# Performance work log

Hardware: AMD Instinct MI355X
Metric: run time of the kernel (lower is better)

The kernel has to match this reference:

```python
import jax, jax.numpy as jnp
import numpy as np

NEG_SLOPE = 0.2  # PyG GATv2Conv default
HEADS = 3


def setup_inputs() -> dict:
    key = jax.random.key(0)
    ks = jax.random.split(key, 5)
    N, D, H, C = 16384, 128, HEADS, 128
    x = jax.random.normal(ks[0], (N, D), dtype=jnp.float32)
    Wl = jax.random.normal(ks[1], (D, H * C), dtype=jnp.float32) * (1.0 / np.sqrt(D))
    Wr = jax.random.normal(ks[2], (D, H * C), dtype=jnp.float32) * (1.0 / np.sqrt(D))
    att = jax.random.normal(ks[3], (H, C), dtype=jnp.float32) * (1.0 / np.sqrt(C))
    bias = jnp.zeros((C,), dtype=jnp.float32)
    return {"x": x, "Wl": Wl, "Wr": Wr, "att": att, "bias": bias, "k": 16}


def _knn_indices(x, k):
    # squared euclidean pairwise distances, exclude self (loop=False)
    sq = jnp.sum(x * x, axis=1)
    dist = sq[:, None] + sq[None, :] - 2.0 * (x @ x.T)  # [N, N]
    n = x.shape[0]
    ar = jnp.arange(n)
    dist = dist.at[ar, ar].set(jnp.inf)
    _, idx = jax.lax.top_k(-dist, k)  # [N, k] neighbor (source) indices per target node
    return idx


def reference(x, Wl, Wr, att, bias, k):
    N = x.shape[0]
    H = att.shape[0]
    C = att.shape[1]
    idx = _knn_indices(x, k)                     # [N, k]
    xl = (x @ Wl).reshape(N, H, C)               # source transform
    xr = (x @ Wr).reshape(N, H, C)               # target transform
    xl_nbr = xl[idx]                             # [N, k, H, C] gathered source feats
    g = jax.nn.leaky_relu(xl_nbr + xr[:, None], NEG_SLOPE)
    e = jnp.einsum('nkhc,hc->nkh', g, att)       # per-edge attention logits
    alpha = jax.nn.softmax(e, axis=1)            # softmax over the k neighbors of each target
    out = jnp.einsum('nkh,nkhc->nhc', alpha, xl_nbr)
    return out.mean(axis=1) + bias               # concat=False: mean over heads, then bias
```

## Files before the change

### kernel.cpp

```cpp
#include <hip/hip_runtime.h>
#include <math.h>

#define N_NODES 16384
#define DIM 128
#define HC 384
#define NEG_SLOPE 0.2f
#define KNN 16
#define KP2 10
#define NSEG 4
#define NCAND 160
#define SEGC (N_NODES / NSEG)
#define TILES64 (SEGC / 64)
#define LROW 272
#define LBUF64 (64 * LROW)

typedef _Float16 f16x8 __attribute__((ext_vector_type(8)));
typedef _Float16 f16x2 __attribute__((ext_vector_type(2)));
typedef float f32x4 __attribute__((ext_vector_type(4)));
typedef unsigned long long u64;

__global__ __launch_bounds__(256) void prep_x(const float* __restrict__ x,
                                              float* __restrict__ sq,
                                              _Float16* __restrict__ xhi,
                                              _Float16* __restrict__ xlo) {
  const int wv = threadIdx.x >> 6;
  const int lane = threadIdx.x & 63;
  const int row = blockIdx.x * 4 + wv;
  const float2 v = *(const float2*)&x[row * DIM + lane * 2];
  float s = v.x * v.x + v.y * v.y;
  #pragma unroll
  for (int off = 32; off > 0; off >>= 1) s += __shfl_down(s, off);
  _Float16 h0 = (_Float16)v.x, h1 = (_Float16)v.y;
  _Float16 l0 = (_Float16)(v.x - (float)h0), l1 = (_Float16)(v.y - (float)h1);
  f16x2 hh; hh[0] = h0; hh[1] = h1;
  f16x2 ll; ll[0] = l0; ll[1] = l1;
  *(f16x2*)&xhi[row * DIM + lane * 2] = hh;
  *(f16x2*)&xlo[row * DIM + lane * 2] = ll;
  if (lane == 0) sq[row] = s;
}

__global__ __launch_bounds__(256) void prep_w(const float* __restrict__ Wl,
                                              const float* __restrict__ Wr,
                                              _Float16* __restrict__ wthi,
                                              _Float16* __restrict__ wtlo) {
  const int t = blockIdx.x * 256 + threadIdx.x;
  const int mat = t / 49152;
  const int e = t - mat * 49152;
  const int k = e / HC;
  const int c = e - k * HC;
  const float w = (mat ? Wr : Wl)[e];
  _Float16 h = (_Float16)w;
  _Float16 l = (_Float16)(w - (float)h);
  wthi[mat * 49152 + c * DIM + k] = h;
  wtlo[mat * 49152 + c * DIM + k] = l;
}

__global__ __launch_bounds__(256) void gemm_xw_mfma(const _Float16* __restrict__ xhi,
                                                    const _Float16* __restrict__ xlo,
                                                    const _Float16* __restrict__ wthi,
                                                    const _Float16* __restrict__ wtlo,
                                                    _Float16* __restrict__ xl,
                                                    _Float16* __restrict__ xr) {
  const int lane = threadIdx.x & 63;
  const int wid = blockIdx.x * 4 + (threadIdx.x >> 6);
  const int mat = wid / 6144;
  const int rem = wid - mat * 6144;
  const int rt = rem / 6;
  const int ctg = rem - rt * 6;
  const int r0 = lane & 15;
  const int g8 = (lane >> 4) * 8;

  const _Float16* ap_hi = xhi + (size_t)(rt * 16 + r0) * DIM + g8;
  const _Float16* ap_lo = xlo + (size_t)(rt * 16 + r0) * DIM + g8;
  f16x8 ah[4], al[4];
  #pragma unroll
  for (int ks = 0; ks < 4; ks++) {
    ah[ks] = *(const f16x8*)(ap_hi + ks * 32);
    al[ks] = *(const f16x8*)(ap_lo + ks * 32);
  }
  _Float16* o = mat ? xr : xl;

  #pragma unroll
  for (int ct4 = 0; ct4 < 4; ct4++) {
    const int ct = ctg * 4 + ct4;
    const _Float16* bp_hi = wthi + mat * 49152 + (ct * 16 + r0) * DIM + g8;
    const _Float16* bp_lo = wtlo + mat * 49152 + (ct * 16 + r0) * DIM + g8;
    f32x4 acc = {0.f, 0.f, 0.f, 0.f};
    #pragma unroll
    for (int ks = 0; ks < 4; ks++) {
      f16x8 bh = *(const f16x8*)(bp_hi + ks * 32);
      f16x8 bl = *(const f16x8*)(bp_lo + ks * 32);
      acc = __builtin_amdgcn_mfma_f32_16x16x32_f16(ah[ks], bh, acc, 0, 0, 0);
      acc = __builtin_amdgcn_mfma_f32_16x16x32_f16(ah[ks], bl, acc, 0, 0, 0);
      acc = __builtin_amdgcn_mfma_f32_16x16x32_f16(al[ks], bh, acc, 0, 0, 0);
    }
    #pragma unroll
    for (int i = 0; i < 4; i++) {
      const int row = rt * 16 + (lane >> 4) * 4 + i;
      o[(size_t)row * HC + ct * 16 + r0] = (_Float16)acc[i];
    }
  }
}

__device__ __forceinline__ unsigned umin32(unsigned a, unsigned b) { return a < b ? a : b; }
__device__ __forceinline__ unsigned umax32(unsigned a, unsigned b) { return a > b ? a : b; }

__device__ __forceinline__ void ripple(unsigned pk, unsigned* pool) {
  unsigned cur = pk;
  #pragma unroll
  for (int s = 0; s < KP2; s++) {
    const unsigned mn = umin32(cur, pool[s]);
    cur = umax32(cur, pool[s]);
    pool[s] = mn;
  }
}

__device__ __forceinline__ void insert4s(const f32x4 acc, const f32x4 scv,
                                         int cb_cg, int selfid, unsigned* pool) {
  unsigned k0, k1, k2, k3;
  {
    unsigned kk[4];
    #pragma unroll
    for (int r = 0; r < 4; r++) {
      const int cid = cb_cg + r;
      const float key = fmaf(-2.f, acc[r], scv[r]);
      unsigned u = __float_as_uint(key);
      u ^= (unsigned)(((int)u >> 31) | 0x80000000u);
      unsigned pk = (u & 0xFFFFC000u) | (unsigned)cid;
      kk[r] = (cid == selfid) ? 0xFFFFFFFFu : pk;
    }
    k0 = kk[0]; k1 = kk[1]; k2 = kk[2]; k3 = kk[3];
  }
  #define CSWAP(a, b) { const unsigned mn = umin32(a, b), mx = umax32(a, b); a = mn; b = mx; }
  CSWAP(k0, k1) CSWAP(k2, k3) CSWAP(k0, k2) CSWAP(k1, k3) CSWAP(k1, k2)
  #undef CSWAP
  ripple(k0, pool);
  if (k1 < pool[KP2 - 1]) {
    ripple(k1, pool);
    ripple(k2, pool);
    ripple(k3, pool);
  }
}

__global__ __launch_bounds__(256) void knn_kernel(const _Float16* __restrict__ xhi,
                                                  const float* __restrict__ sq,
                                                  int* __restrict__ cand) {
  __shared__ __align__(16) char lds[2 * LBUF64];

  const int lane = threadIdx.x & 63;
  const int w = threadIdx.x >> 6;
  const int seg = __builtin_amdgcn_readfirstlane(blockIdx.x & 3);
  const int rowgroup = __builtin_amdgcn_readfirstlane((blockIdx.x >> 2) * 4 + w);
  const int rowbase = rowgroup * 16;
  const int segbase = seg * SEGC;
  const int r0 = lane & 15;
  const int g8 = (lane >> 4) * 8;
  const int cg4 = (lane >> 4) * 4;
  const int selfid = rowbase + r0;

  const int st_row = 4 * w + (lane >> 4);
  const int st_chunk = lane & 15;
  size_t st_src[4];
  char* st_dst[4];
  #pragma unroll
  for (int k = 0; k < 4; k++) {
    st_src[k] = (size_t)(st_row + 16 * k) * DIM + st_chunk * 8;
    st_dst[k] = &lds[(st_row + 16 * k) * LROW + st_chunk * 16];
  }

  f16x8 b[4];
  {
    const size_t rb = (size_t)(rowbase + r0) * DIM + g8;
    #pragma unroll
    for (int ks = 0; ks < 4; ks++) b[ks] = *(const f16x8*)&xhi[rb + ks * 32];
  }

  unsigned pool[KP2];
  #pragma unroll
  for (int j = 0; j < KP2; j++) pool[j] = 0xFFFFFFFFu;

  {
    const size_t tb = (size_t)segbase * DIM;
    #pragma unroll
    for (int k = 0; k < 4; k++)
      *(float4*)(st_dst[k]) = *(const float4*)&xhi[tb + st_src[k]];
  }
  f32x4 sA[4];
  #pragma unroll
  for (int s = 0; s < 4; s++) sA[s] = *(const f32x4*)&sq[segbase + 16 * s + cg4];
  __syncthreads();

  int cur = 0;
  for (int t = 0; t < TILES64; t++) {
    const int tn = (t + 1) & (TILES64 - 1);
    const size_t nb = (size_t)(segbase + tn * 64) * DIM;
    float4 g[4];
    #pragma unroll
    for (int k = 0; k < 4; k++) g[k] = *(const float4*)&xhi[nb + st_src[k]];
    f32x4 sN[4];
    #pragma unroll
    for (int s = 0; s < 4; s++) sN[s] = *(const f32x4*)&sq[segbase + tn * 64 + 16 * s + cg4];

    const int cb = segbase + t * 64;
    #pragma unroll
    for (int pr = 0; pr < 2; pr++) {
      const int s0 = pr * 2, s1 = pr * 2 + 1;
      const char* rb0 = &lds[cur * LBUF64 + (16 * s0 + r0) * LROW + g8 * 2];
      const char* rb1 = &lds[cur * LBUF64 + (16 * s1 + r0) * LROW + g8 * 2];
      f16x8 a0[4], a1[4];
      #pragma unroll
      for (int ks = 0; ks < 4; ks++) {
        a0[ks] = *(const f16x8*)(rb0 + ks * 64);
        a1[ks] = *(const f16x8*)(rb1 + ks * 64);
      }
      f32x4 acc0 = {0.f, 0.f, 0.f, 0.f};
      f32x4 acc1 = {0.f, 0.f, 0.f, 0.f};
      #pragma unroll
      for (int ks = 0; ks < 4; ks++) {
        acc0 = __builtin_amdgcn_mfma_f32_16x16x32_f16(a0[ks], b[ks], acc0, 0, 0, 0);
        acc1 = __builtin_amdgcn_mfma_f32_16x16x32_f16(a1[ks], b[ks], acc1, 0, 0, 0);
      }
      insert4s(acc0, sA[s0], cb + 16 * s0 + cg4, selfid, pool);
      insert4s(acc1, sA[s1], cb + 16 * s1 + cg4, selfid, pool);
    }

    #pragma unroll
    for (int k = 0; k < 4; k++)
      *(float4*)(st_dst[k] + (cur ^ 1) * LBUF64) = g[k];
    __syncthreads();
    #pragma unroll
    for (int s = 0; s < 4; s++) sA[s] = sN[s];
    cur ^= 1;
  }

  const int row = rowbase + r0;
  int* dst = cand + (size_t)row * NCAND + ((lane >> 4) * NSEG + seg) * KP2;
  #pragma unroll
  for (int e = 0; e < KP2; e++) dst[e] = (int)(pool[e] & 0x3FFFu);
}

__device__ __forceinline__ unsigned flip32(float f) {
  unsigned u = __float_as_uint(f);
  return u ^ (unsigned)(((int)u >> 31) | 0x80000000u);
}
__device__ __forceinline__ u64 umin64(u64 a, u64 b) { return a < b ? a : b; }

__global__ __launch_bounds__(256) void refine_kernel(const float* __restrict__ x,
                                                     const float* __restrict__ sq,
                                                     const int* __restrict__ cand,
                                                     int* __restrict__ idxo) {
  __shared__ __align__(16) float Xrow[4][DIM];
  __shared__ u64 Keys[4][NCAND];
  const int wv = threadIdx.x >> 6;
  const int lane = threadIdx.x & 63;
  const int row = blockIdx.x * 4 + wv;

  {
    const float2 v = *(const float2*)&x[(size_t)row * DIM + lane * 2];
    *(float2*)&Xrow[wv][lane * 2] = v;
  }

  const int cs = lane >> 3;
  const int ch8 = lane & 7;
  const int base = row * NCAND;
  const float sr = sq[row];

  #pragma nounroll
  for (int it = 0; it < 20; it++) {
    const int ci = it * 8 + cs;
    const int c = cand[base + ci];
    const float4* p = (const float4*)&x[(size_t)c * DIM];
    float d = 0.f;
    #pragma unroll
    for (int j = 0; j < 4; j++) {
      const float4 a = p[ch8 + 8 * j];
      const float4 xv = *(const float4*)&Xrow[wv][(ch8 + 8 * j) * 4];
      d += xv.x * a.x + xv.y * a.y + xv.z * a.z + xv.w * a.w;
    }
    d += __shfl_xor(d, 1);
    d += __shfl_xor(d, 2);
    d += __shfl_xor(d, 4);
    if (ch8 == 0) {
      const float dist = sr + sq[c] - 2.f * d;
      Keys[wv][ci] = ((u64)flip32(dist) << 32) | (unsigned)c;
    }
  }

  u64 k0 = Keys[wv][lane];
  u64 k1 = Keys[wv][64 + lane];
  u64 k2 = (lane < 32) ? Keys[wv][128 + lane] : ~0ull;

  int* dst = idxo + (size_t)row * KNN;
  #pragma unroll
  for (int e = 0; e < KNN; e++) {
    u64 m = umin64(k0, umin64(k1, k2));
    #pragma unroll
    for (int off = 32; off > 0; off >>= 1) {
      const u64 o = __shfl_xor(m, off);
      m = umin64(m, o);
    }
    if (k0 == m)      { dst[e] = (int)(unsigned)m; k0 = ~0ull; }
    else if (k1 == m) { dst[e] = (int)(unsigned)m; k1 = ~0ull; }
    else if (k2 == m) { dst[e] = (int)(unsigned)m; k2 = ~0ull; }
  }
}

__global__ __launch_bounds__(256) void attn_kernel(const _Float16* __restrict__ xl,
                                                   const _Float16* __restrict__ xr,
                                                   const float* __restrict__ att,
                                                   const float* __restrict__ bias,
                                                   const int* __restrict__ idxo,
                                                   float* __restrict__ out) {
  const int n = blockIdx.x * 4 + (threadIdx.x >> 6);
  const int lane = threadIdx.x & 63;
  const int ch = lane * 2;
  int myn = 0;
  if (lane < KNN) myn = idxo[(size_t)n * KNN + lane];
  float o0 = 0.f, o1 = 0.f;
  #pragma unroll
  for (int h = 0; h < 3; h++) {
    const f16x2 rr = *(const f16x2*)&xr[(size_t)n * HC + h * 128 + ch];
    const float r0 = (float)rr[0], r1 = (float)rr[1];
    const float2 av = *(const float2*)&att[h * 128 + ch];
    float v0[KNN], v1[KNN], e[KNN];
    #pragma unroll
    for (int kk = 0; kk < KNN; kk++) {
      const f16x2 xv = *(const f16x2*)&xl[(size_t)__shfl(myn, kk) * HC + h * 128 + ch];
      const float x0 = (float)xv[0], x1 = (float)xv[1];
      v0[kk] = x0; v1[kk] = x1;
      float g0 = x0 + r0; g0 = g0 >= 0.f ? g0 : NEG_SLOPE * g0;
      float g1 = x1 + r1; g1 = g1 >= 0.f ? g1 : NEG_SLOPE * g1;
      float p = av.x * g0 + av.y * g1;
      #pragma unroll
      for (int off = 32; off > 0; off >>= 1) p += __shfl_xor(p, off);
      e[kk] = p;
    }
    float m = e[0];
    #pragma unroll
    for (int kk = 1; kk < KNN; kk++) m = fmaxf(m, e[kk]);
    float s = 0.f;
    float w[KNN];
    #pragma unroll
    for (int kk = 0; kk < KNN; kk++) { w[kk] = expf(e[kk] - m); s += w[kk]; }
    #pragma unroll
    for (int kk = 0; kk < KNN; kk++) {
      const float al = w[kk] / s;
      o0 += al * v0[kk];
      o1 += al * v1[kk];
    }
  }
  const float2 bv = *(const float2*)&bias[ch];
  float2 ov;
  ov.x = o0 / 3.f + bv.x;
  ov.y = o1 / 3.f + bv.y;
  *(float2*)&out[(size_t)n * 128 + ch] = ov;
}

extern "C" void kernel_launch(void* const* d_in, const int* in_sizes, int n_in,
                              void* d_out, int out_size, void* d_ws, size_t ws_size,
                              hipStream_t stream) {
  const float* x    = (const float*)d_in[0];
  const float* Wl   = (const float*)d_in[1];
  const float* Wr   = (const float*)d_in[2];
  const float* att  = (const float*)d_in[3];
  const float* bias = (const float*)d_in[4];
  float* out = (float*)d_out;

  _Float16* xhi  = (_Float16*)d_ws;
  _Float16* xlo  = xhi + (size_t)N_NODES * DIM;
  _Float16* wthi = xlo + (size_t)N_NODES * DIM;
  _Float16* wtlo = wthi + 2 * HC * DIM;
  _Float16* xl   = wtlo + 2 * HC * DIM;
  _Float16* xr   = xl + (size_t)N_NODES * HC;
  float*    sqv  = (float*)(xr + (size_t)N_NODES * HC);
  int*      cnd  = (int*)(sqv + N_NODES);
  int*      idx  = cnd + (size_t)N_NODES * NCAND;

  prep_x<<<N_NODES / 4, 256, 0, stream>>>(x, sqv, xhi, xlo);
  prep_w<<<384, 256, 0, stream>>>(Wl, Wr, wthi, wtlo);
  gemm_xw_mfma<<<3072, 256, 0, stream>>>(xhi, xlo, wthi, wtlo, xl, xr);
  knn_kernel<<<N_NODES / 16, 256, 0, stream>>>(xhi, sqv, cnd);
  refine_kernel<<<N_NODES / 4, 256, 0, stream>>>(x, sqv, cnd, idx);
  attn_kernel<<<N_NODES / 4, 256, 0, stream>>>(xl, xr, att, bias, idx, out);
}
```

Measured before the change: 421.3 us.

## Register-block KNN over two row tiles per wave and share A-fragments in projection GEMM

```diff
diff --git a/kernel.cpp b/kernel.cpp
--- a/kernel.cpp
+++ b/kernel.cpp
@@ -6,9 +6,9 @@
 #define HC 384
 #define NEG_SLOPE 0.2f
 #define KNN 16
-#define KP2 10
-#define NSEG 4
-#define NCAND 160
+#define KP2 6
+#define NSEG 8
+#define NCAND 192
 #define SEGC (N_NODES / NSEG)
 #define TILES64 (SEGC / 64)
 #define LROW 272
@@ -63,10 +63,8 @@
                                                     _Float16* __restrict__ xr) {
   const int lane = threadIdx.x & 63;
   const int wid = blockIdx.x * 4 + (threadIdx.x >> 6);
-  const int mat = wid / 6144;
-  const int rem = wid - mat * 6144;
-  const int rt = rem / 6;
-  const int ctg = rem - rt * 6;
+  const int rt = wid / 6;
+  const int ctg = wid - rt * 6;
   const int r0 = lane & 15;
   const int g8 = (lane >> 4) * 8;
 
@@ -78,26 +76,29 @@
     ah[ks] = *(const f16x8*)(ap_hi + ks * 32);
     al[ks] = *(const f16x8*)(ap_lo + ks * 32);
   }
-  _Float16* o = mat ? xr : xl;
-
-  #pragma unroll
-  for (int ct4 = 0; ct4 < 4; ct4++) {
-    const int ct = ctg * 4 + ct4;
-    const _Float16* bp_hi = wthi + mat * 49152 + (ct * 16 + r0) * DIM + g8;
-    const _Float16* bp_lo = wtlo + mat * 49152 + (ct * 16 + r0) * DIM + g8;
-    f32x4 acc = {0.f, 0.f, 0.f, 0.f};
-    #pragma unroll
-    for (int ks = 0; ks < 4; ks++) {
-      f16x8 bh = *(const f16x8*)(bp_hi + ks * 32);
-      f16x8 bl = *(const f16x8*)(bp_lo + ks * 32);
-      acc = __builtin_amdgcn_mfma_f32_16x16x32_f16(ah[ks], bh, acc, 0, 0, 0);
-      acc = __builtin_amdgcn_mfma_f32_16x16x32_f16(ah[ks], bl, acc, 0, 0, 0);
-      acc = __builtin_amdgcn_mfma_f32_16x16x32_f16(al[ks], bh, acc, 0, 0, 0);
-    }
-    #pragma unroll
-    for (int i = 0; i < 4; i++) {
-      const int row = rt * 16 + (lane >> 4) * 4 + i;
-      o[(size_t)row * HC + ct * 16 + r0] = (_Float16)acc[i];
+
+  #pragma unroll
+  for (int mat = 0; mat < 2; mat++) {
+    _Float16* o = mat ? xr : xl;
+    #pragma unroll
+    for (int ct4 = 0; ct4 < 4; ct4++) {
+      const int ct = ctg * 4 + ct4;
+      const _Float16* bp_hi = wthi + mat * 49152 + (ct * 16 + r0) * DIM + g8;
+      const _Float16* bp_lo = wtlo + mat * 49152 + (ct * 16 + r0) * DIM + g8;
+      f32x4 acc = {0.f, 0.f, 0.f, 0.f};
+      #pragma unroll
+      for (int ks = 0; ks < 4; ks++) {
+        f16x8 bh = *(const f16x8*)(bp_hi + ks * 32);
+        f16x8 bl = *(const f16x8*)(bp_lo + ks * 32);
+        acc = __builtin_amdgcn_mfma_f32_16x16x32_f16(ah[ks], bh, acc, 0, 0, 0);
+        acc = __builtin_amdgcn_mfma_f32_16x16x32_f16(ah[ks], bl, acc, 0, 0, 0);
+        acc = __builtin_amdgcn_mfma_f32_16x16x32_f16(al[ks], bh, acc, 0, 0, 0);
+      }
+      #pragma unroll
+      for (int i = 0; i < 4; i++) {
+        const int row = rt * 16 + (lane >> 4) * 4 + i;
+        o[(size_t)row * HC + ct * 16 + r0] = (_Float16)acc[i];
+      }
     }
   }
 }
@@ -142,21 +143,22 @@
   }
 }
 
-__global__ __launch_bounds__(256) void knn_kernel(const _Float16* __restrict__ xhi,
-                                                  const float* __restrict__ sq,
-                                                  int* __restrict__ cand) {
+__global__ __launch_bounds__(256, 4) void knn_kernel(const _Float16* __restrict__ xhi,
+                                                     const float* __restrict__ sq,
+                                                     int* __restrict__ cand) {
   __shared__ __align__(16) char lds[2 * LBUF64];
 
   const int lane = threadIdx.x & 63;
   const int w = threadIdx.x >> 6;
-  const int seg = __builtin_amdgcn_readfirstlane(blockIdx.x & 3);
-  const int rowgroup = __builtin_amdgcn_readfirstlane((blockIdx.x >> 2) * 4 + w);
-  const int rowbase = rowgroup * 16;
+  const int seg = __builtin_amdgcn_readfirstlane(blockIdx.x & 7);
+  const int blockrow = __builtin_amdgcn_readfirstlane(blockIdx.x >> 3);
+  const int rowbase = blockrow * 128 + w * 32;
   const int segbase = seg * SEGC;
   const int r0 = lane & 15;
   const int g8 = (lane >> 4) * 8;
   const int cg4 = (lane >> 4) * 4;
-  const int selfid = rowbase + r0;
+  const int selfid0 = rowbase + r0;
+  const int selfid1 = rowbase + 16 + r0;
 
   const int st_row = 4 * w + (lane >> 4);
   const int st_chunk = lane & 15;
@@ -168,16 +170,20 @@
     st_dst[k] = &lds[(st_row + 16 * k) * LROW + st_chunk * 16];
   }
 
-  f16x8 b[4];
+  f16x8 b_lo[4], b_hi[4];
   {
-    const size_t rb = (size_t)(rowbase + r0) * DIM + g8;
-    #pragma unroll
-    for (int ks = 0; ks < 4; ks++) b[ks] = *(const f16x8*)&xhi[rb + ks * 32];
-  }
-
-  unsigned pool[KP2];
-  #pragma unroll
-  for (int j = 0; j < KP2; j++) pool[j] = 0xFFFFFFFFu;
+    const size_t rb0 = (size_t)(rowbase + r0) * DIM + g8;
+    const size_t rb1 = (size_t)(rowbase + 16 + r0) * DIM + g8;
+    #pragma unroll
+    for (int ks = 0; ks < 4; ks++) {
+      b_lo[ks] = *(const f16x8*)&xhi[rb0 + ks * 32];
+      b_hi[ks] = *(const f16x8*)&xhi[rb1 + ks * 32];
+    }
+  }
+
+  unsigned pool0[KP2], pool1[KP2];
+  #pragma unroll
+  for (int j = 0; j < KP2; j++) { pool0[j] = 0xFFFFFFFFu; pool1[j] = 0xFFFFFFFFu; }
 
   {
     const size_t tb = (size_t)segbase * DIM;
@@ -213,15 +219,21 @@
         a0[ks] = *(const f16x8*)(rb0 + ks * 64);
         a1[ks] = *(const f16x8*)(rb1 + ks * 64);
       }
-      f32x4 acc0 = {0.f, 0.f, 0.f, 0.f};
-      f32x4 acc1 = {0.f, 0.f, 0.f, 0.f};
+      f32x4 acc00 = {0.f, 0.f, 0.f, 0.f};
+      f32x4 acc01 = {0.f, 0.f, 0.f, 0.f};
+      f32x4 acc10 = {0.f, 0.f, 0.f, 0.f};
+      f32x4 acc11 = {0.f, 0.f, 0.f, 0.f};
       #pragma unroll
       for (int ks = 0; ks < 4; ks++) {
-        acc0 = __builtin_amdgcn_mfma_f32_16x16x32_f16(a0[ks], b[ks], acc0, 0, 0, 0);
-        acc1 = __builtin_amdgcn_mfma_f32_16x16x32_f16(a1[ks], b[ks], acc1, 0, 0, 0);
+        acc00 = __builtin_amdgcn_mfma_f32_16x16x32_f16(a0[ks], b_lo[ks], acc00, 0, 0, 0);
+        acc01 = __builtin_amdgcn_mfma_f32_16x16x32_f16(a0[ks], b_hi[ks], acc01, 0, 0, 0);
+        acc10 = __builtin_amdgcn_mfma_f32_16x16x32_f16(a1[ks], b_lo[ks], acc10, 0, 0, 0);
+        acc11 = __builtin_amdgcn_mfma_f32_16x16x32_f16(a1[ks], b_hi[ks], acc11, 0, 0, 0);
       }
-      insert4s(acc0, sA[s0], cb + 16 * s0 + cg4, selfid, pool);
-      insert4s(acc1, sA[s1], cb + 16 * s1 + cg4, selfid, pool);
+      insert4s(acc00, sA[s0], cb + 16 * s0 + cg4, selfid0, pool0);
+      insert4s(acc01, sA[s0], cb + 16 * s0 + cg4, selfid1, pool1);
+      insert4s(acc10, sA[s1], cb + 16 * s1 + cg4, selfid0, pool0);
+      insert4s(acc11, sA[s1], cb + 16 * s1 + cg4, selfid1, pool1);
     }
 
     #pragma unroll
@@ -233,10 +245,14 @@
     cur ^= 1;
   }
 
-  const int row = rowbase + r0;
-  int* dst = cand + (size_t)row * NCAND + ((lane >> 4) * NSEG + seg) * KP2;
-  #pragma unroll
-  for (int e = 0; e < KP2; e++) dst[e] = (int)(pool[e] & 0x3FFFu);
+  const int slot = ((lane >> 4) * NSEG + seg) * KP2;
+  int* dst0 = cand + (size_t)(rowbase + r0) * NCAND + slot;
+  int* dst1 = cand + (size_t)(rowbase + 16 + r0) * NCAND + slot;
+  #pragma unroll
+  for (int e = 0; e < KP2; e++) {
+    dst0[e] = (int)(pool0[e] & 0x3FFFu);
+    dst1[e] = (int)(pool1[e] & 0x3FFFu);
+  }
 }
 
 __device__ __forceinline__ unsigned flip32(float f) {
@@ -266,7 +282,7 @@
   const float sr = sq[row];
 
   #pragma nounroll
-  for (int it = 0; it < 20; it++) {
+  for (int it = 0; it < NCAND / 8; it++) {
     const int ci = it * 8 + cs;
     const int c = cand[base + ci];
     const float4* p = (const float4*)&x[(size_t)c * DIM];
@@ -288,7 +304,7 @@
 
   u64 k0 = Keys[wv][lane];
   u64 k1 = Keys[wv][64 + lane];
-  u64 k2 = (lane < 32) ? Keys[wv][128 + lane] : ~0ull;
+  u64 k2 = Keys[wv][128 + lane];
 
   int* dst = idxo + (size_t)row * KNN;
   #pragma unroll
@@ -378,8 +394,8 @@
 
   prep_x<<<N_NODES / 4, 256, 0, stream>>>(x, sqv, xhi, xlo);
   prep_w<<<384, 256, 0, stream>>>(Wl, Wr, wthi, wtlo);
-  gemm_xw_mfma<<<3072, 256, 0, stream>>>(xhi, xlo, wthi, wtlo, xl, xr);
-  knn_kernel<<<N_NODES / 16, 256, 0, stream>>>(xhi, sqv, cnd);
+  gemm_xw_mfma<<<1536, 256, 0, stream>>>(xhi, xlo, wthi, wtlo, xl, xr);
+  knn_kernel<<<(N_NODES / 128) * NSEG, 256, 0, stream>>>(xhi, sqv, cnd);
   refine_kernel<<<N_NODES / 4, 256, 0, stream>>>(x, sqv, cnd, idx);
   attn_kernel<<<N_NODES / 4, 256, 0, stream>>>(xl, xr, att, bias, idx, out);
 }
```

Result: faster. 376.9 us (-10.6%).
